# Kernel tuning notes

Hardware: AMD Instinct MI355X
Metric: run time of the kernel (lower is better)

Reference implementation:

```python
import jax, jax.numpy as jnp
import numpy as np

MIN_RES, MAX_RES, NUM_LOD, BAND_WIDTH = 6, 64, 10, 10
CODEBOOK_SIZE = 2 ** BAND_WIDTH
FEAT_DIM = 3
N_PTS = 2_000_000
_b = np.exp((np.log(MAX_RES) - np.log(MIN_RES)) / (NUM_LOD - 1))
LODS = [int(1 + np.floor(MIN_RES * _b ** l)) for l in range(NUM_LOD)]
# Instant-NGP spatial hash primes
PRIMES = np.array([1, 2654435761, 805459861], dtype=np.uint32)
# 8 corner offsets of a voxel
OFFSETS = np.array([[i, j, k] for i in (0, 1) for j in (0, 1) for k in (0, 1)], dtype=np.int32)  # [8,3]


def setup_inputs() -> dict:
    key = jax.random.key(0)
    keys = jax.random.split(key, NUM_LOD + 1)
    pts = jax.random.uniform(keys[0], (N_PTS, 3), dtype=jnp.float32)  # points in [0,1]^3
    inp = {"pts": pts}
    for i, lod in enumerate(LODS):
        size = min(lod ** 2, CODEBOOK_SIZE)
        inp[f"codebook_{i}"] = 0.01 * jax.random.normal(keys[i + 1], (size, FEAT_DIM), dtype=jnp.float32)
    return inp


def _trilinear_hash(res, codebook, pts):
    # pts: [N,3] in [0,1]; scale to grid of `res` vertices per axis
    x = pts * (res - 1)
    x0 = jnp.clip(jnp.floor(x).astype(jnp.int32), 0, res - 2)  # [N,3]
    w = x - x0.astype(x.dtype)                                  # [N,3] fractional
    corners = x0[:, None, :] + jnp.asarray(OFFSETS)[None]       # [N,8,3]
    cu = corners.astype(jnp.uint32)
    size = codebook.shape[0]
    h = (cu[..., 0] * jnp.uint32(PRIMES[0])) ^ (cu[..., 1] * jnp.uint32(PRIMES[1])) ^ (cu[..., 2] * jnp.uint32(PRIMES[2]))
    idx = (h % jnp.uint32(size)).astype(jnp.int32)              # [N,8]
    feats = codebook[idx]                                       # [N,8,F] gather
    c = jnp.asarray(OFFSETS, dtype=x.dtype)                     # [8,3]
    # trilinear weight per corner: prod_d (c_d ? w_d : 1-w_d)
    wc = jnp.prod(c[None] * w[:, None, :] + (1.0 - c[None]) * (1.0 - w[:, None, :]), axis=-1)  # [N,8]
    return jnp.einsum('nkf,nk->nf', feats, wc)                  # [N,F]


def reference(pts, codebook_0, codebook_1, codebook_2, codebook_3, codebook_4,
              codebook_5, codebook_6, codebook_7, codebook_8, codebook_9):
    codebooks = [codebook_0, codebook_1, codebook_2, codebook_3, codebook_4,
                 codebook_5, codebook_6, codebook_7, codebook_8, codebook_9]
    out = jnp.zeros((pts.shape[0], FEAT_DIM), dtype=pts.dtype)
    for res, cb in zip(LODS, codebooks):  # cat(...,-1).sum(-1) == sum over levels
        out = out + _trilinear_hash(res, cb, pts)
    return out
```

## Files before the change

kernel.cpp:

```cpp
#include <hip/hip_runtime.h>
#include <hip/hip_fp16.h>
#include <cmath>

#define NLOD 10

static constexpr int SIZES[NLOD]     = {49, 64, 121, 196, 324, 529, 900, 1024, 1024, 1024};
static constexpr int ENTRY_OFS[NLOD] = {0, 49, 113, 234, 430, 754, 1283, 2183, 3207, 4231};
static constexpr int TOTAL_ENTRIES   = 5255;

struct ResArr { int r[NLOD]; };

template <int SIZE>
__device__ __forceinline__ void level_accum(const __half* __restrict__ cb, int res,
                                            float px, float py, float pz,
                                            float& a0, float& a1, float& a2)
{
    constexpr bool POW2 = (SIZE & (SIZE - 1)) == 0;
    constexpr unsigned P1 = 2654435761u, P2 = 805459861u;

    const float s = (float)(res - 1);
    float fx = px * s, fy = py * s, fz = pz * s;

    float gx = floorf(fx), gy = floorf(fy), gz = floorf(fz);
    float wx = fx - gx, wy = fy - gy, wz = fz - gz;

    unsigned ux = (unsigned)(int)gx;
    unsigned uy = (unsigned)(int)gy;
    unsigned uz = (unsigned)(int)gz;

    unsigned hx0, hx1, hy0, hy1, hz0, hz1;
    if constexpr (POW2) {
        hx0 = ux << 3;        hx1 = hx0 + 8u;
        hy0 = uy * (P1 * 8u); hy1 = hy0 + (P1 * 8u);
        hz0 = uz * (P2 * 8u); hz1 = hz0 + (P2 * 8u);
    } else {
        hx0 = ux;       hx1 = ux + 1u;
        hy0 = uy * P1;  hy1 = hy0 + P1;
        hz0 = uz * P2;  hz1 = hz0 + P2;
    }
    unsigned h00 = hx0 ^ hy0, h01 = hx0 ^ hy1;
    unsigned h10 = hx1 ^ hy0, h11 = hx1 ^ hy1;

    float wx0 = 1.0f - wx, wy0 = 1.0f - wy, wz0 = 1.0f - wz;
    float w00 = wx0 * wy0, w01 = wx0 * wy, w10 = wx * wy0, w11 = wx * wy;

    auto corner = [&](unsigned h, float wt) {
        uint2 raw;
        if constexpr (POW2) {
            unsigned addr = h & (unsigned)((SIZE - 1) * 8);
            raw = *reinterpret_cast<const uint2*>(reinterpret_cast<const char*>(cb) + addr);
        } else {
            unsigned idx = h % (unsigned)SIZE;
            raw = reinterpret_cast<const uint2*>(cb)[idx];
        }
        asm("v_fma_mix_f32 %0, %1, %2, %0 op_sel_hi:[1,0,0]"
            : "+v"(a0) : "v"(raw.x), "v"(wt));
        asm("v_fma_mix_f32 %0, %1, %2, %0 op_sel:[1,0,0] op_sel_hi:[1,0,0]"
            : "+v"(a1) : "v"(raw.x), "v"(wt));
        asm("v_fma_mix_f32 %0, %1, %2, %0 op_sel_hi:[1,0,0]"
            : "+v"(a2) : "v"(raw.y), "v"(wt));
    };

    corner(h00 ^ hz0, w00 * wz0);
    corner(h00 ^ hz1, w00 * wz);
    corner(h01 ^ hz0, w01 * wz0);
    corner(h01 ^ hz1, w01 * wz);
    corner(h10 ^ hz0, w10 * wz0);
    corner(h10 ^ hz1, w10 * wz);
    corner(h11 ^ hz0, w11 * wz0);
    corner(h11 ^ hz1, w11 * wz);
}

__global__ __launch_bounds__(1024, 8)
void hashgrid_kernel(const float* __restrict__ pts,
                     const float* __restrict__ c0, const float* __restrict__ c1,
                     const float* __restrict__ c2, const float* __restrict__ c3,
                     const float* __restrict__ c4, const float* __restrict__ c5,
                     const float* __restrict__ c6, const float* __restrict__ c7,
                     const float* __restrict__ c8, const float* __restrict__ c9,
                     float* __restrict__ out, int npts, ResArr res)
{
    __shared__ __half cbh[TOTAL_ENTRIES * 4];

    {
        const float* srcs[NLOD] = {c0, c1, c2, c3, c4, c5, c6, c7, c8, c9};
#pragma unroll
        for (int L = 0; L < NLOD; ++L) {
            for (int e = threadIdx.x; e < SIZES[L]; e += blockDim.x) {
                const float* s = srcs[L] + e * 3;
                __half2* d = reinterpret_cast<__half2*>(cbh + (ENTRY_OFS[L] + e) * 4);
                d[0] = __floats2half2_rn(s[0], s[1]);
                d[1] = __floats2half2_rn(s[2], 0.0f);
            }
        }
    }
    __syncthreads();

    const int S = gridDim.x * blockDim.x;
    for (int n = blockIdx.x * blockDim.x + threadIdx.x; n < npts; n += 2 * S) {
        const int m = n + S;
        const bool hasB = (m < npts);
        const int mc = hasB ? m : n;

        float ax = pts[n * 3 + 0], ay = pts[n * 3 + 1], az = pts[n * 3 + 2];
        float bx = pts[mc * 3 + 0], by = pts[mc * 3 + 1], bz = pts[mc * 3 + 2];

        float A0 = 0.0f, A1 = 0.0f, A2 = 0.0f;
        float B0 = 0.0f, B1 = 0.0f, B2 = 0.0f;

#define LEVEL2(SZ, L)                                                              \
        level_accum<SZ>(cbh + ENTRY_OFS[L] * 4, res.r[L], ax, ay, az, A0, A1, A2); \
        level_accum<SZ>(cbh + ENTRY_OFS[L] * 4, res.r[L], bx, by, bz, B0, B1, B2);

        LEVEL2(  49, 0)
        LEVEL2(  64, 1)
        LEVEL2( 121, 2)
        LEVEL2( 196, 3)
        LEVEL2( 324, 4)
        LEVEL2( 529, 5)
        LEVEL2( 900, 6)
        LEVEL2(1024, 7)
        LEVEL2(1024, 8)
        LEVEL2(1024, 9)
#undef LEVEL2

        out[n * 3 + 0] = A0;
        out[n * 3 + 1] = A1;
        out[n * 3 + 2] = A2;
        if (hasB) {
            out[m * 3 + 0] = B0;
            out[m * 3 + 1] = B1;
            out[m * 3 + 2] = B2;
        }
    }
}

extern "C" void kernel_launch(void* const* d_in, const int* in_sizes, int n_in,
                              void* d_out, int out_size, void* d_ws, size_t ws_size,
                              hipStream_t stream)
{
    const float* pts = (const float*)d_in[0];
    const int npts = in_sizes[0] / 3;

    ResArr ra;
    const double b = exp((log(64.0) - log(6.0)) / 9.0);
    for (int l = 0; l < NLOD; ++l)
        ra.r[l] = (int)(1.0 + floor(6.0 * pow(b, (double)l)));

    hashgrid_kernel<<<dim3(512), dim3(1024), 0, stream>>>(
        pts,
        (const float*)d_in[1], (const float*)d_in[2], (const float*)d_in[3],
        (const float*)d_in[4], (const float*)d_in[5], (const float*)d_in[6],
        (const float*)d_in[7], (const float*)d_in[8], (const float*)d_in[9],
        (const float*)d_in[10],
        (float*)d_out, npts, ra);
}
```

Before: 139.4 us.

## Move last two hash levels from LDS to global fp16 tables via pack kernel

The two finest 1024-entry codebooks are no longer staged in shared memory. A small pre-kernel packs them to fp16 in the workspace, and the main kernel gathers them from global memory, where they should stay cache-resident. This cuts the per-block LDS footprint and the per-block staging work, and splits random gathers between LDS and the vector memory path. The cost is an extra kernel launch and higher-latency global/L1 gathers for 16 of the 80 corner lookups per point.

```diff
diff --git a/kernel.cpp b/kernel.cpp
--- a/kernel.cpp
+++ b/kernel.cpp
@@ -1,19 +1,23 @@
 #include <hip/hip_runtime.h>
 #include <hip/hip_fp16.h>
 #include <cmath>
+#include <cstdint>
 
 #define NLOD 10
 
 static constexpr int SIZES[NLOD]     = {49, 64, 121, 196, 324, 529, 900, 1024, 1024, 1024};
 static constexpr int ENTRY_OFS[NLOD] = {0, 49, 113, 234, 430, 754, 1283, 2183, 3207, 4231};
-static constexpr int TOTAL_ENTRIES   = 5255;
+static constexpr int LDS_ENTRIES = 3207;
 
 struct ResArr { int r[NLOD]; };
 
+struct LevelCtx {
+    unsigned h00, h01, h10, h11, hz0, hz1;
+    float w00z0, w00z1, w01z0, w01z1, w10z0, w10z1, w11z0, w11z1;
+};
+
 template <int SIZE>
-__device__ __forceinline__ void level_accum(const __half* __restrict__ cb, int res,
-                                            float px, float py, float pz,
-                                            float& a0, float& a1, float& a2)
+__device__ __forceinline__ LevelCtx level_ctx(int res, float px, float py, float pz)
 {
     constexpr bool POW2 = (SIZE & (SIZE - 1)) == 0;
     constexpr unsigned P1 = 2654435761u, P2 = 805459861u;
@@ -28,21 +32,47 @@
     unsigned uy = (unsigned)(int)gy;
     unsigned uz = (unsigned)(int)gz;
 
-    unsigned hx0, hx1, hy0, hy1, hz0, hz1;
+    LevelCtx c;
+    unsigned hx0, hx1, hy0, hy1;
     if constexpr (POW2) {
         hx0 = ux << 3;        hx1 = hx0 + 8u;
         hy0 = uy * (P1 * 8u); hy1 = hy0 + (P1 * 8u);
-        hz0 = uz * (P2 * 8u); hz1 = hz0 + (P2 * 8u);
+        c.hz0 = uz * (P2 * 8u); c.hz1 = c.hz0 + (P2 * 8u);
     } else {
         hx0 = ux;       hx1 = ux + 1u;
         hy0 = uy * P1;  hy1 = hy0 + P1;
-        hz0 = uz * P2;  hz1 = hz0 + P2;
+        c.hz0 = uz * P2; c.hz1 = c.hz0 + P2;
     }
-    unsigned h00 = hx0 ^ hy0, h01 = hx0 ^ hy1;
-    unsigned h10 = hx1 ^ hy0, h11 = hx1 ^ hy1;
+    c.h00 = hx0 ^ hy0; c.h01 = hx0 ^ hy1;
+    c.h10 = hx1 ^ hy0; c.h11 = hx1 ^ hy1;
 
     float wx0 = 1.0f - wx, wy0 = 1.0f - wy, wz0 = 1.0f - wz;
     float w00 = wx0 * wy0, w01 = wx0 * wy, w10 = wx * wy0, w11 = wx * wy;
+    c.w00z0 = w00 * wz0; c.w00z1 = w00 * wz;
+    c.w01z0 = w01 * wz0; c.w01z1 = w01 * wz;
+    c.w10z0 = w10 * wz0; c.w10z1 = w10 * wz;
+    c.w11z0 = w11 * wz0; c.w11z1 = w11 * wz;
+    return c;
+}
+
+__device__ __forceinline__ void acc3(uint2 raw, float wt,
+                                     float& a0, float& a1, float& a2)
+{
+    asm("v_fma_mix_f32 %0, %1, %2, %0 op_sel_hi:[1,0,0]"
+        : "+v"(a0) : "v"(raw.x), "v"(wt));
+    asm("v_fma_mix_f32 %0, %1, %2, %0 op_sel:[1,0,0] op_sel_hi:[1,0,0]"
+        : "+v"(a1) : "v"(raw.x), "v"(wt));
+    asm("v_fma_mix_f32 %0, %1, %2, %0 op_sel_hi:[1,0,0]"
+        : "+v"(a2) : "v"(raw.y), "v"(wt));
+}
+
+template <int SIZE>
+__device__ __forceinline__ void level_lds(const __half* __restrict__ cb, int res,
+                                          float px, float py, float pz,
+                                          float& a0, float& a1, float& a2)
+{
+    constexpr bool POW2 = (SIZE & (SIZE - 1)) == 0;
+    LevelCtx c = level_ctx<SIZE>(res, px, py, pz);
 
     auto corner = [&](unsigned h, float wt) {
         uint2 raw;
@@ -53,22 +83,49 @@
             unsigned idx = h % (unsigned)SIZE;
             raw = reinterpret_cast<const uint2*>(cb)[idx];
         }
-        asm("v_fma_mix_f32 %0, %1, %2, %0 op_sel_hi:[1,0,0]"
-            : "+v"(a0) : "v"(raw.x), "v"(wt));
-        asm("v_fma_mix_f32 %0, %1, %2, %0 op_sel:[1,0,0] op_sel_hi:[1,0,0]"
-            : "+v"(a1) : "v"(raw.x), "v"(wt));
-        asm("v_fma_mix_f32 %0, %1, %2, %0 op_sel_hi:[1,0,0]"
-            : "+v"(a2) : "v"(raw.y), "v"(wt));
+        acc3(raw, wt, a0, a1, a2);
     };
 
-    corner(h00 ^ hz0, w00 * wz0);
-    corner(h00 ^ hz1, w00 * wz);
-    corner(h01 ^ hz0, w01 * wz0);
-    corner(h01 ^ hz1, w01 * wz);
-    corner(h10 ^ hz0, w10 * wz0);
-    corner(h10 ^ hz1, w10 * wz);
-    corner(h11 ^ hz0, w11 * wz0);
-    corner(h11 ^ hz1, w11 * wz);
+    corner(c.h00 ^ c.hz0, c.w00z0);
+    corner(c.h00 ^ c.hz1, c.w00z1);
+    corner(c.h01 ^ c.hz0, c.w01z0);
+    corner(c.h01 ^ c.hz1, c.w01z1);
+    corner(c.h10 ^ c.hz0, c.w10z0);
+    corner(c.h10 ^ c.hz1, c.w10z1);
+    corner(c.h11 ^ c.hz0, c.w11z0);
+    corner(c.h11 ^ c.hz1, c.w11z1);
+}
+
+__device__ __forceinline__ void level_g(const char* __restrict__ cb, int res,
+                                        float px, float py, float pz,
+                                        float& a0, float& a1, float& a2)
+{
+    LevelCtx c = level_ctx<1024>(res, px, py, pz);
+
+    auto corner = [&](unsigned h, float wt) {
+        unsigned addr = h & (unsigned)(1023 * 8);
+        uint2 raw = *reinterpret_cast<const uint2*>(cb + addr);
+        acc3(raw, wt, a0, a1, a2);
+    };
+
+    corner(c.h00 ^ c.hz0, c.w00z0);
+    corner(c.h00 ^ c.hz1, c.w00z1);
+    corner(c.h01 ^ c.hz0, c.w01z0);
+    corner(c.h01 ^ c.hz1, c.w01z1);
+    corner(c.h10 ^ c.hz0, c.w10z0);
+    corner(c.h10 ^ c.hz1, c.w10z1);
+    corner(c.h11 ^ c.hz0, c.w11z0);
+    corner(c.h11 ^ c.hz1, c.w11z1);
+}
+
+__global__ void pack_kernel(const float* __restrict__ c8,
+                            const float* __restrict__ c9,
+                            __half2* __restrict__ ws)
+{
+    int t = blockIdx.x * blockDim.x + threadIdx.x;
+    const float* src = (t < 1024) ? (c8 + t * 3) : (c9 + (t - 1024) * 3);
+    ws[t * 2 + 0] = __floats2half2_rn(src[0], src[1]);
+    ws[t * 2 + 1] = __floats2half2_rn(src[2], 0.0f);
 }
 
 __global__ __launch_bounds__(1024, 8)
@@ -77,15 +134,15 @@
                      const float* __restrict__ c2, const float* __restrict__ c3,
                      const float* __restrict__ c4, const float* __restrict__ c5,
                      const float* __restrict__ c6, const float* __restrict__ c7,
-                     const float* __restrict__ c8, const float* __restrict__ c9,
+                     const char* __restrict__ g8, const char* __restrict__ g9,
                      float* __restrict__ out, int npts, ResArr res)
 {
-    __shared__ __half cbh[TOTAL_ENTRIES * 4];
+    __shared__ __half cbh[LDS_ENTRIES * 4];
 
     {
-        const float* srcs[NLOD] = {c0, c1, c2, c3, c4, c5, c6, c7, c8, c9};
+        const float* srcs[8] = {c0, c1, c2, c3, c4, c5, c6, c7};
 #pragma unroll
-        for (int L = 0; L < NLOD; ++L) {
+        for (int L = 0; L < 8; ++L) {
             for (int e = threadIdx.x; e < SIZES[L]; e += blockDim.x) {
                 const float* s = srcs[L] + e * 3;
                 __half2* d = reinterpret_cast<__half2*>(cbh + (ENTRY_OFS[L] + e) * 4);
@@ -108,9 +165,9 @@
         float A0 = 0.0f, A1 = 0.0f, A2 = 0.0f;
         float B0 = 0.0f, B1 = 0.0f, B2 = 0.0f;
 
-#define LEVEL2(SZ, L)                                                              \
-        level_accum<SZ>(cbh + ENTRY_OFS[L] * 4, res.r[L], ax, ay, az, A0, A1, A2); \
-        level_accum<SZ>(cbh + ENTRY_OFS[L] * 4, res.r[L], bx, by, bz, B0, B1, B2);
+#define LEVEL2(SZ, L)                                                             \
+        level_lds<SZ>(cbh + ENTRY_OFS[L] * 4, res.r[L], ax, ay, az, A0, A1, A2);  \
+        level_lds<SZ>(cbh + ENTRY_OFS[L] * 4, res.r[L], bx, by, bz, B0, B1, B2);
 
         LEVEL2(  49, 0)
         LEVEL2(  64, 1)
@@ -120,9 +177,11 @@
         LEVEL2( 529, 5)
         LEVEL2( 900, 6)
         LEVEL2(1024, 7)
-        LEVEL2(1024, 8)
-        LEVEL2(1024, 9)
 #undef LEVEL2
+        level_g(g8, res.r[8], ax, ay, az, A0, A1, A2);
+        level_g(g8, res.r[8], bx, by, bz, B0, B1, B2);
+        level_g(g9, res.r[9], ax, ay, az, A0, A1, A2);
+        level_g(g9, res.r[9], bx, by, bz, B0, B1, B2);
 
         out[n * 3 + 0] = A0;
         out[n * 3 + 1] = A1;
@@ -147,11 +206,17 @@
     for (int l = 0; l < NLOD; ++l)
         ra.r[l] = (int)(1.0 + floor(6.0 * pow(b, (double)l)));
 
+    pack_kernel<<<dim3(8), dim3(256), 0, stream>>>(
+        (const float*)d_in[9], (const float*)d_in[10], (__half2*)d_ws);
+
+    const char* g8 = (const char*)d_ws;
+    const char* g9 = (const char*)d_ws + 8192;
+
     hashgrid_kernel<<<dim3(512), dim3(1024), 0, stream>>>(
         pts,
         (const float*)d_in[1], (const float*)d_in[2], (const float*)d_in[3],
         (const float*)d_in[4], (const float*)d_in[5], (const float*)d_in[6],
-        (const float*)d_in[7], (const float*)d_in[8], (const float*)d_in[9],
-        (const float*)d_in[10],
+        (const float*)d_in[7], (const float*)d_in[8],
+        g8, g9,
         (float*)d_out, npts, ra);
 }
```

After: 143.2 us. +2.7%, slower.

## Move two codebooks to global fp16 buffer and software-pipeline level loads

Applied to the files above, without the earlier changes.

Levels 8 and 9 are packed to fp16 by a separate pre-kernel into workspace and read through global/L1 instead of LDS. This shrinks LDS per block, allowing smaller 512-thread blocks with more resident blocks. The per-point loop now handles one point instead of two, with loads for level L+1 issued before consuming level L through double-buffered register arrays. Point loads and output stores use nontemporal hints. The risks are an extra kernel launch, cache-based global gathers for the largest levels, and higher register pressure from the double buffering.

```diff
diff --git a/kernel.cpp b/kernel.cpp
--- a/kernel.cpp
+++ b/kernel.cpp
@@ -1,19 +1,31 @@
 #include <hip/hip_runtime.h>
 #include <hip/hip_fp16.h>
 #include <cmath>
+#include <cstdint>
 
 #define NLOD 10
 
 static constexpr int SIZES[NLOD]     = {49, 64, 121, 196, 324, 529, 900, 1024, 1024, 1024};
 static constexpr int ENTRY_OFS[NLOD] = {0, 49, 113, 234, 430, 754, 1283, 2183, 3207, 4231};
-static constexpr int TOTAL_ENTRIES   = 5255;
+static constexpr int LDS_ENTRIES = 3207;
 
 struct ResArr { int r[NLOD]; };
 
-template <int SIZE>
-__device__ __forceinline__ void level_accum(const __half* __restrict__ cb, int res,
-                                            float px, float py, float pz,
-                                            float& a0, float& a1, float& a2)
+__device__ __forceinline__ void acc3(uint2 raw, float wt,
+                                     float& a0, float& a1, float& a2)
+{
+    asm("v_fma_mix_f32 %0, %1, %2, %0 op_sel_hi:[1,0,0]"
+        : "+v"(a0) : "v"(raw.x), "v"(wt));
+    asm("v_fma_mix_f32 %0, %1, %2, %0 op_sel:[1,0,0] op_sel_hi:[1,0,0]"
+        : "+v"(a1) : "v"(raw.x), "v"(wt));
+    asm("v_fma_mix_f32 %0, %1, %2, %0 op_sel_hi:[1,0,0]"
+        : "+v"(a2) : "v"(raw.y), "v"(wt));
+}
+
+template <int SIZE, bool GLOBAL>
+__device__ __forceinline__ void load_level(const char* __restrict__ cb, int res,
+                                           float px, float py, float pz,
+                                           uint2 (&r)[8], float (&w)[8])
 {
     constexpr bool POW2 = (SIZE & (SIZE - 1)) == 0;
     constexpr unsigned P1 = 2654435761u, P2 = 805459861u;
@@ -41,51 +53,63 @@
     unsigned h00 = hx0 ^ hy0, h01 = hx0 ^ hy1;
     unsigned h10 = hx1 ^ hy0, h11 = hx1 ^ hy1;
 
+    auto fetch = [&](unsigned h) -> uint2 {
+        unsigned addr;
+        if constexpr (POW2) addr = h & (unsigned)((SIZE - 1) * 8);
+        else                addr = (h % (unsigned)SIZE) * 8u;
+        return *reinterpret_cast<const uint2*>(cb + addr);
+    };
+
+    r[0] = fetch(h00 ^ hz0);
+    r[1] = fetch(h00 ^ hz1);
+    r[2] = fetch(h01 ^ hz0);
+    r[3] = fetch(h01 ^ hz1);
+    r[4] = fetch(h10 ^ hz0);
+    r[5] = fetch(h10 ^ hz1);
+    r[6] = fetch(h11 ^ hz0);
+    r[7] = fetch(h11 ^ hz1);
+
     float wx0 = 1.0f - wx, wy0 = 1.0f - wy, wz0 = 1.0f - wz;
     float w00 = wx0 * wy0, w01 = wx0 * wy, w10 = wx * wy0, w11 = wx * wy;
-
-    auto corner = [&](unsigned h, float wt) {
-        uint2 raw;
-        if constexpr (POW2) {
-            unsigned addr = h & (unsigned)((SIZE - 1) * 8);
-            raw = *reinterpret_cast<const uint2*>(reinterpret_cast<const char*>(cb) + addr);
-        } else {
-            unsigned idx = h % (unsigned)SIZE;
-            raw = reinterpret_cast<const uint2*>(cb)[idx];
-        }
-        asm("v_fma_mix_f32 %0, %1, %2, %0 op_sel_hi:[1,0,0]"
-            : "+v"(a0) : "v"(raw.x), "v"(wt));
-        asm("v_fma_mix_f32 %0, %1, %2, %0 op_sel:[1,0,0] op_sel_hi:[1,0,0]"
-            : "+v"(a1) : "v"(raw.x), "v"(wt));
-        asm("v_fma_mix_f32 %0, %1, %2, %0 op_sel_hi:[1,0,0]"
-            : "+v"(a2) : "v"(raw.y), "v"(wt));
-    };
-
-    corner(h00 ^ hz0, w00 * wz0);
-    corner(h00 ^ hz1, w00 * wz);
-    corner(h01 ^ hz0, w01 * wz0);
-    corner(h01 ^ hz1, w01 * wz);
-    corner(h10 ^ hz0, w10 * wz0);
-    corner(h10 ^ hz1, w10 * wz);
-    corner(h11 ^ hz0, w11 * wz0);
-    corner(h11 ^ hz1, w11 * wz);
+    w[0] = w00 * wz0; w[1] = w00 * wz;
+    w[2] = w01 * wz0; w[3] = w01 * wz;
+    w[4] = w10 * wz0; w[5] = w10 * wz;
+    w[6] = w11 * wz0; w[7] = w11 * wz;
 }
 
-__global__ __launch_bounds__(1024, 8)
+__device__ __forceinline__ void consume(const uint2 (&r)[8], const float (&w)[8],
+                                        float& a0, float& a1, float& a2)
+{
+#pragma unroll
+    for (int k = 0; k < 8; ++k)
+        acc3(r[k], w[k], a0, a1, a2);
+}
+
+__global__ void pack_kernel(const float* __restrict__ c8,
+                            const float* __restrict__ c9,
+                            __half2* __restrict__ ws)
+{
+    int t = blockIdx.x * blockDim.x + threadIdx.x;
+    const float* src = (t < 1024) ? (c8 + t * 3) : (c9 + (t - 1024) * 3);
+    ws[t * 2 + 0] = __floats2half2_rn(src[0], src[1]);
+    ws[t * 2 + 1] = __floats2half2_rn(src[2], 0.0f);
+}
+
+__global__ __launch_bounds__(512, 6)
 void hashgrid_kernel(const float* __restrict__ pts,
                      const float* __restrict__ c0, const float* __restrict__ c1,
                      const float* __restrict__ c2, const float* __restrict__ c3,
                      const float* __restrict__ c4, const float* __restrict__ c5,
                      const float* __restrict__ c6, const float* __restrict__ c7,
-                     const float* __restrict__ c8, const float* __restrict__ c9,
+                     const char* __restrict__ g8, const char* __restrict__ g9,
                      float* __restrict__ out, int npts, ResArr res)
 {
-    __shared__ __half cbh[TOTAL_ENTRIES * 4];
+    __shared__ __half cbh[LDS_ENTRIES * 4];
 
     {
-        const float* srcs[NLOD] = {c0, c1, c2, c3, c4, c5, c6, c7, c8, c9};
+        const float* srcs[8] = {c0, c1, c2, c3, c4, c5, c6, c7};
 #pragma unroll
-        for (int L = 0; L < NLOD; ++L) {
+        for (int L = 0; L < 8; ++L) {
             for (int e = threadIdx.x; e < SIZES[L]; e += blockDim.x) {
                 const float* s = srcs[L] + e * 3;
                 __half2* d = reinterpret_cast<__half2*>(cbh + (ENTRY_OFS[L] + e) * 4);
@@ -96,42 +120,47 @@
     }
     __syncthreads();
 
+    const char* lds = reinterpret_cast<const char*>(cbh);
+
     const int S = gridDim.x * blockDim.x;
-    for (int n = blockIdx.x * blockDim.x + threadIdx.x; n < npts; n += 2 * S) {
-        const int m = n + S;
-        const bool hasB = (m < npts);
-        const int mc = hasB ? m : n;
+    for (int n = blockIdx.x * blockDim.x + threadIdx.x; n < npts; n += S) {
+        float px = __builtin_nontemporal_load(pts + n * 3 + 0);
+        float py = __builtin_nontemporal_load(pts + n * 3 + 1);
+        float pz = __builtin_nontemporal_load(pts + n * 3 + 2);
 
-        float ax = pts[n * 3 + 0], ay = pts[n * 3 + 1], az = pts[n * 3 + 2];
-        float bx = pts[mc * 3 + 0], by = pts[mc * 3 + 1], bz = pts[mc * 3 + 2];
+        float a0 = 0.0f, a1 = 0.0f, a2 = 0.0f;
 
-        float A0 = 0.0f, A1 = 0.0f, A2 = 0.0f;
-        float B0 = 0.0f, B1 = 0.0f, B2 = 0.0f;
+        uint2 rA[8], rB[8];
+        float wA[8], wB[8];
 
-#define LEVEL2(SZ, L)                                                              \
-        level_accum<SZ>(cbh + ENTRY_OFS[L] * 4, res.r[L], ax, ay, az, A0, A1, A2); \
-        level_accum<SZ>(cbh + ENTRY_OFS[L] * 4, res.r[L], bx, by, bz, B0, B1, B2);
+#define LD(L, SZ, GLB, BASE, R, W) \
+        load_level<SZ, GLB>(BASE, res.r[L], px, py, pz, R, W);
 
-        LEVEL2(  49, 0)
-        LEVEL2(  64, 1)
-        LEVEL2( 121, 2)
-        LEVEL2( 196, 3)
-        LEVEL2( 324, 4)
-        LEVEL2( 529, 5)
-        LEVEL2( 900, 6)
-        LEVEL2(1024, 7)
-        LEVEL2(1024, 8)
-        LEVEL2(1024, 9)
-#undef LEVEL2
+        LD(0,   49, false, lds + ENTRY_OFS[0] * 8, rA, wA)
+        LD(1,   64, false, lds + ENTRY_OFS[1] * 8, rB, wB)
+        consume(rA, wA, a0, a1, a2);
+        LD(2,  121, false, lds + ENTRY_OFS[2] * 8, rA, wA)
+        consume(rB, wB, a0, a1, a2);
+        LD(3,  196, false, lds + ENTRY_OFS[3] * 8, rB, wB)
+        consume(rA, wA, a0, a1, a2);
+        LD(4,  324, false, lds + ENTRY_OFS[4] * 8, rA, wA)
+        consume(rB, wB, a0, a1, a2);
+        LD(5,  529, false, lds + ENTRY_OFS[5] * 8, rB, wB)
+        consume(rA, wA, a0, a1, a2);
+        LD(6,  900, false, lds + ENTRY_OFS[6] * 8, rA, wA)
+        consume(rB, wB, a0, a1, a2);
+        LD(7, 1024, false, lds + ENTRY_OFS[7] * 8, rB, wB)
+        consume(rA, wA, a0, a1, a2);
+        LD(8, 1024, true,  g8,                     rA, wA)
+        consume(rB, wB, a0, a1, a2);
+        LD(9, 1024, true,  g9,                     rB, wB)
+        consume(rA, wA, a0, a1, a2);
+        consume(rB, wB, a0, a1, a2);
+#undef LD
 
-        out[n * 3 + 0] = A0;
-        out[n * 3 + 1] = A1;
-        out[n * 3 + 2] = A2;
-        if (hasB) {
-            out[m * 3 + 0] = B0;
-            out[m * 3 + 1] = B1;
-            out[m * 3 + 2] = B2;
-        }
+        __builtin_nontemporal_store(a0, out + n * 3 + 0);
+        __builtin_nontemporal_store(a1, out + n * 3 + 1);
+        __builtin_nontemporal_store(a2, out + n * 3 + 2);
     }
 }
 
@@ -147,11 +176,17 @@
     for (int l = 0; l < NLOD; ++l)
         ra.r[l] = (int)(1.0 + floor(6.0 * pow(b, (double)l)));
 
-    hashgrid_kernel<<<dim3(512), dim3(1024), 0, stream>>>(
+    pack_kernel<<<dim3(8), dim3(256), 0, stream>>>(
+        (const float*)d_in[9], (const float*)d_in[10], (__half2*)d_ws);
+
+    const char* g8 = (const char*)d_ws;
+    const char* g9 = (const char*)d_ws + 8192;
+
+    hashgrid_kernel<<<dim3(768), dim3(512), 0, stream>>>(
         pts,
         (const float*)d_in[1], (const float*)d_in[2], (const float*)d_in[3],
         (const float*)d_in[4], (const float*)d_in[5], (const float*)d_in[6],
-        (const float*)d_in[7], (const float*)d_in[8], (const float*)d_in[9],
-        (const float*)d_in[10],
+        (const float*)d_in[7], (const float*)d_in[8],
+        g8, g9,
         (float*)d_out, npts, ra);
 }
```

Measured after the change: 148.3 us. 6.4% more time.
